# Kernel tuning notes

Measured on AMD Instinct MI355X. Metric: run time of the kernel, lower is better.

The kernel has to match this reference:

```python
import jax, jax.numpy as jnp
import numpy as np

N, E = 10000, 160000
D, H, C, FF, L = 128, 4, 32, 512, 2
INNER = H * C
VOCAB, RELVOCAB = 32000, 100
EPS = 1e-6
GATE_BIAS = 3.0


def _layer_norm(x, w, b):
    mu = jnp.mean(x, axis=-1, keepdims=True)
    var = jnp.mean(jnp.square(x - mu), axis=-1, keepdims=True)
    return (x - mu) * jax.lax.rsqrt(var + EPS) * w + b


def setup_inputs() -> dict:
    key = jax.random.key(0)
    ks = jax.random.split(key, 24)
    s = 1.0 / np.sqrt(D)
    inp = {
        "node_ids": jax.random.randint(ks[0], (N,), 0, VOCAB),
        "edge_index": jax.random.randint(ks[1], (2, E), 0, N),
        "edge_ids": jax.random.randint(ks[2], (E,), 0, RELVOCAB),
        "node_emb": jax.random.normal(ks[3], (VOCAB, D), jnp.float32),
        "edge_emb": jax.random.normal(ks[4], (RELVOCAB, D), jnp.float32),
        # per-layer stacked params (torch Linear weight layout [out, in])
        "ln_w": jnp.ones((L, D), jnp.float32),
        "ln_b": jnp.zeros((L, D), jnp.float32),
        "q_w": jax.random.normal(ks[5], (L, INNER, D), jnp.float32) * (1.0 / np.sqrt(D * C)),
        "relA_w": jax.random.normal(ks[6], (L, FF, 2 * D), jnp.float32) * s,
        "relA_b": jnp.zeros((L, FF), jnp.float32),
        "relB_w": jax.random.normal(ks[7], (L, D, FF), jnp.float32) * s,
        "relB_b": jnp.zeros((L, D), jnp.float32),
        "relG_w": jax.random.normal(ks[8], (L, D, FF), jnp.float32) * s,
        "relG_b": jnp.zeros((L, D), jnp.float32),
        "k_w": jax.random.normal(ks[9], (L, INNER, 2 * D), jnp.float32) * s,
        "v_w": jax.random.normal(ks[10], (L, INNER, D), jnp.float32) * s,
        "o_w": jax.random.normal(ks[11], (L, D, INNER), jnp.float32) * (1.0 / np.sqrt(INNER)),
        "ff_ln_w": jnp.ones((L, D), jnp.float32),
        "ff_ln_b": jnp.zeros((L, D), jnp.float32),
        "wi_w": jax.random.normal(ks[12], (L, FF, D), jnp.float32) * s,
        "wo_w": jax.random.normal(ks[13], (L, D, FF), jnp.float32) * (1.0 / np.sqrt(FF)),
    }
    return inp


def _forward(node_ids, edge_index, edge_ids, node_emb, edge_emb, ln_w, ln_b,
             q_w, relA_w, relA_b, relB_w, relB_b, relG_w, relG_b,
             k_w, v_w, o_w, ff_ln_w, ff_ln_b, wi_w, wo_w):
    x = node_emb[node_ids]          # [N, D]
    ef = edge_emb[edge_ids]         # [E, D]
    src = edge_index[0]             # j (source / kv side)
    dst = edge_index[1]             # i (target / query side)
    for l in range(L):
        # --- relational self-attention ---
        q = _layer_norm(x, ln_w[l], ln_b[l])
        q = (q @ q_w[l].T).reshape(N, H, C)
        kv_j = x[src]                                   # [E, D]
        cat = jnp.concatenate([kv_j, ef], axis=-1)      # [E, 2D]
        inter = jax.nn.celu(cat @ relA_w[l].T + relA_b[l])   # [E, FF]
        gate = jax.nn.sigmoid(inter @ relG_w[l].T + relG_b[l] + GATE_BIAS)
        k_add = inter @ relB_w[l].T + relB_b[l]
        kv2 = kv_j * gate + k_add * (1.0 - gate)        # [E, D]
        k = (jnp.concatenate([kv2, ef], axis=-1) @ k_w[l].T).reshape(E, H, C)
        v = (kv2 @ v_w[l].T).reshape(E, H, C)
        scores = jnp.sum(q[dst] * k, axis=-1)           # [E, H]
        smax = jax.ops.segment_max(scores, dst, num_segments=N)
        ex = jnp.exp(scores - smax[dst])
        denom = jax.ops.segment_sum(ex, dst, num_segments=N)
        alpha = ex / denom[dst]                         # [E, H]
        msg = (v * alpha[..., None]).reshape(E, INNER)
        agg = jax.ops.segment_sum(msg, dst, num_segments=N)  # [N, INNER]
        x = x + agg @ o_w[l].T
        # --- feed-forward (T5-style, pre-LN, relu, residual) ---
        h = _layer_norm(x, ff_ln_w[l], ff_ln_b[l])
        x = x + jax.nn.relu(h @ wi_w[l].T) @ wo_w[l].T
    return x


def reference(node_ids, edge_index, edge_ids, node_emb, edge_emb, ln_w, ln_b,
              q_w, relA_w, relA_b, relB_w, relB_b, relG_w, relG_b,
              k_w, v_w, o_w, ff_ln_w, ff_ln_b, wi_w, wo_w):
    return _forward(node_ids, edge_index, edge_ids, node_emb, edge_emb, ln_w, ln_b,
                    q_w, relA_w, relA_b, relB_w, relB_b, relG_w, relG_b,
                    k_w, v_w, o_w, ff_ln_w, ff_ln_b, wi_w, wo_w)
```

## Files before the change

kernel.cpp:

```cpp
#include <hip/hip_runtime.h>
#include <hip/hip_bf16.h>

#define NN 10000
#define EE 160000
#define DD 128
#define HH 4
#define CC 32
#define FFF 512
#define LL 2
#define RELV 100
#define EPS 1e-6f
#define GATE_BIAS 3.0f
#define BM 32
#define NT 16

typedef __bf16 bf16x8 __attribute__((ext_vector_type(8)));
typedef float f32x4 __attribute__((ext_vector_type(4)));
typedef float f32x16 __attribute__((ext_vector_type(16)));

#define MFMA(a,b,c)   __builtin_amdgcn_mfma_f32_16x16x32_bf16((a),(b),(c),0,0,0)
#define MFMA32(a,b,c) __builtin_amdgcn_mfma_f32_32x32x16_bf16((a),(b),(c),0,0,0)

__device__ __forceinline__ int swzK(int e, int b){ return e*256 + (b ^ ((e&7)<<4)); }
__device__ __forceinline__ int swz128(int e, int b){ return e*256 + (b ^ ((e&7)<<4)); }
__device__ __forceinline__ int swz512(int e, int b){ return e*1024 + (b ^ ((e&7)<<4)); }

__global__ __launch_bounds__(256) void k_gx(
    const int* __restrict__ node_ids, const float* __restrict__ node_emb,
    float* __restrict__ x, ushort* __restrict__ xb,
    const int* __restrict__ dst, int* __restrict__ hist){
  int b = blockIdx.x, t = threadIdx.x;
  int n = b*2 + (t>>7);
  int c = t & 127;
  float v = node_emb[(long)node_ids[n]*DD + c];
  x[(long)n*DD + c] = v;
  __hip_bfloat16 h = __float2bfloat16(v);
  xb[(long)n*DD + c] = *(ushort*)&h;
  if (t < 32){
    int e = b*32 + t;
    atomicAdd(&hist[dst[e]], 1);
  }
}

__device__ __forceinline__ void wprep_one(
    const float* __restrict__ in, ushort* __restrict__ out, int tid, int IN, int instride){
  int lane = tid & 63;
  int grp  = tid >> 6;
  int nkb  = IN >> 4;
  int kb   = grp % nkb;
  int cb   = grp / nkb;
  int col  = cb*32 + (lane & 31);
  int k0   = kb*16 + (lane >> 5)*8;
  const float* p = in + (long)col*instride + k0;
  bf16x8 h;
  #pragma unroll
  for (int j=0;j<8;++j) h[j] = (__bf16)p[j];
  *(bf16x8*)(out + (long)tid*8) = h;
}

__global__ __launch_bounds__(256) void k_prep(
    const float* __restrict__ relG_w, const float* __restrict__ relB_w,
    const float* __restrict__ k_w, const float* __restrict__ v_w,
    const float* __restrict__ relA_w,
    ushort* __restrict__ Gwb, ushort* __restrict__ Bwb,
    ushort* __restrict__ Kwb, ushort* __restrict__ Vwb, ushort* __restrict__ A1b){
  int tid = blockIdx.x*256 + threadIdx.x;
  if (tid < DD*FFF/8){
    wprep_one(relG_w, Gwb, tid, FFF, FFF);
    wprep_one(relB_w, Bwb, tid, FFF, FFF);
  }
  if (tid < DD*DD/8){
    wprep_one(k_w, Kwb, tid, DD, 256);
    wprep_one(v_w, Vwb, tid, DD, DD);
  }
  {
    int o = tid / DD, i = tid % DD;
    __hip_bfloat16 h = __float2bfloat16(relA_w[(long)o*256 + i]);
    A1b[tid] = *(ushort*)&h;
  }
}

__global__ __launch_bounds__(256) void k_f2b4(
    const float* __restrict__ q_w, const float* __restrict__ o_w,
    const float* __restrict__ wi_w, const float* __restrict__ wo_w,
    ushort* __restrict__ Qwb, ushort* __restrict__ Owb,
    ushort* __restrict__ Wib, ushort* __restrict__ Wob){
  long i = (long)blockIdx.x*256 + threadIdx.x;
  const long nV = (long)LL*DD*DD;
  if (i < nV){
    __hip_bfloat16 h1 = __float2bfloat16(q_w[i]); Qwb[i] = *(ushort*)&h1;
    __hip_bfloat16 h2 = __float2bfloat16(o_w[i]); Owb[i] = *(ushort*)&h2;
  }
  {
    __hip_bfloat16 h3 = __float2bfloat16(wi_w[i]); Wib[i] = *(ushort*)&h3;
    __hip_bfloat16 h4 = __float2bfloat16(wo_w[i]); Wob[i] = *(ushort*)&h4;
  }
}

__global__ __launch_bounds__(256) void k_ea(
    const float* __restrict__ edge_emb, const float* __restrict__ relA_w,
    const float* __restrict__ relA_b, const float* __restrict__ k_w,
    ushort* __restrict__ EA2b, float* __restrict__ EKf){
  int rel = blockIdx.x, t = threadIdx.x;
  __shared__ float emb[128];
  if (t < 128) emb[t] = edge_emb[(long)rel*DD + t];
  __syncthreads();
  for (int f=t; f<FFF; f+=256){
    const float* wr = relA_w + (long)f*256 + 128;
    float s = relA_b[f];
    for (int i=0;i<128;++i) s += emb[i]*wr[i];
    __hip_bfloat16 h = __float2bfloat16(s);
    EA2b[(long)rel*FFF + f] = *(ushort*)&h;
  }
  if (t < 128){
    const float* wr = k_w + (long)t*256 + 128;
    float s = 0.f;
    for (int i=0;i<128;++i) s += emb[i]*wr[i];
    EKf[(long)rel*DD + t] = s;
  }
}

__global__ __launch_bounds__(256) void k_scan(const int* __restrict__ hist, int* __restrict__ cursor){
  __shared__ int tsum[256];
  const int t = threadIdx.x;
  const int PER = (NN + 255) / 256;
  const int base = t*PER;
  int s = 0;
  for (int i=0;i<PER;++i){ int idx = base+i; if (idx < NN) s += hist[idx]; }
  tsum[t] = s;
  __syncthreads();
  if (t == 0){
    int run = 0;
    for (int i=0;i<256;++i){ int v = tsum[i]; tsum[i] = run; run += v; }
  }
  __syncthreads();
  int run = tsum[t];
  for (int i=0;i<PER;++i){
    int idx = base+i;
    if (idx < NN){ int v = hist[idx]; cursor[idx] = run; run += v; }
  }
}
__global__ __launch_bounds__(256) void k_scatter(const int* __restrict__ dst,
    int* __restrict__ cursor, int* __restrict__ perm){
  int e = blockIdx.x*256 + threadIdx.x;
  if (e < EE){
    int p = atomicAdd(&cursor[dst[e]], 1);
    perm[p] = e;
  }
}

__global__ __launch_bounds__(256) void k_lnq_xa(
    const float* __restrict__ x, const float* __restrict__ lnw, const float* __restrict__ lnb,
    const ushort* __restrict__ qwb, const ushort* __restrict__ a1b,
    float* __restrict__ q, ushort* __restrict__ XAb,
    float* __restrict__ agg, float* __restrict__ denom){
  __shared__ __align__(16) unsigned char HB[NT*256];
  __shared__ __align__(16) unsigned char HR[NT*256];
  const int n0 = blockIdx.x*NT;
  const int t = threadIdx.x;
  const int e = t>>4, s = t&15;
  const int w = t>>6, l = t&63, lr = l&15, lg = l>>4;
  {
    float4 z4 = {0.f,0.f,0.f,0.f};
    float* ap = agg + (long)n0*DD + t*8;
    *(float4*)ap = z4; *(float4*)(ap+4) = z4;
    if (t < NT*HH) denom[n0*HH + t] = 0.f;
  }
  {
    const float* xp = x + (long)(n0+e)*DD + s*8;
    float xv[8];
    *(float4*)&xv[0] = *(const float4*)xp;
    *(float4*)&xv[4] = *(const float4*)(xp+4);
    float sm = 0.f;
    #pragma unroll
    for (int i=0;i<8;++i) sm += xv[i];
    sm += __shfl_xor(sm,1); sm += __shfl_xor(sm,2);
    sm += __shfl_xor(sm,4); sm += __shfl_xor(sm,8);
    float mu = sm*(1.f/DD);
    float sq = 0.f;
    #pragma unroll
    for (int i=0;i<8;++i){ float d = xv[i]-mu; sq += d*d; }
    sq += __shfl_xor(sq,1); sq += __shfl_xor(sq,2);
    sq += __shfl_xor(sq,4); sq += __shfl_xor(sq,8);
    float rstd = rsqrtf(sq*(1.f/DD) + EPS);
    float4 w0 = *(const float4*)(lnw + s*8), w1 = *(const float4*)(lnw + s*8 + 4);
    float4 b0 = *(const float4*)(lnb + s*8), b1 = *(const float4*)(lnb + s*8 + 4);
    float wv[8] = {w0.x,w0.y,w0.z,w0.w,w1.x,w1.y,w1.z,w1.w};
    float bv[8] = {b0.x,b0.y,b0.z,b0.w,b1.x,b1.y,b1.z,b1.w};
    bf16x8 hb, hr;
    #pragma unroll
    for (int i=0;i<8;++i){
      hb[i] = (__bf16)((xv[i]-mu)*rstd*wv[i] + bv[i]);
      hr[i] = (__bf16)xv[i];
    }
    *(bf16x8*)(HB + swz128(e, s*16)) = hb;
    *(bf16x8*)(HR + swz128(e, s*16)) = hr;
  }
  __syncthreads();
  {
    const int o0 = w*32;
    f32x4 z = {0.f,0.f,0.f,0.f};
    f32x4 acc[2] = {z,z};
    #pragma unroll
    for (int k4=0;k4<4;++k4){
      bf16x8 a = *(const bf16x8*)(HB + swz128(lr, k4*64 + lg*16));
      #pragma unroll
      for (int nt=0;nt<2;++nt){
        bf16x8 b = *(const bf16x8*)(qwb + (long)(o0+nt*16+lr)*128 + k4*32 + lg*8);
        acc[nt] = MFMA(a, b, acc[nt]);
      }
    }
    #pragma unroll
    for (int nt=0;nt<2;++nt)
      #pragma unroll
      for (int r=0;r<4;++r)
        q[(long)(n0 + lg*4 + r)*DD + o0 + nt*16 + lr] = acc[nt][r];
  }
  {
    const int f0w = w*128;
    f32x4 z = {0.f,0.f,0.f,0.f};
    f32x4 acc[8] = {z,z,z,z,z,z,z,z};
    #pragma unroll
    for (int k4=0;k4<4;++k4){
      bf16x8 a = *(const bf16x8*)(HR + swz128(lr, k4*64 + lg*16));
      #pragma unroll
      for (int nt=0;nt<8;++nt){
        bf16x8 b = *(const bf16x8*)(a1b + (long)(f0w+nt*16+lr)*128 + k4*32 + lg*8);
        acc[nt] = MFMA(a, b, acc[nt]);
      }
    }
    #pragma unroll
    for (int nt=0;nt<8;++nt)
      #pragma unroll
      for (int r=0;r<4;++r){
        __hip_bfloat16 h = __float2bfloat16(acc[nt][r]);
        XAb[(long)(n0+lg*4+r)*FFF + f0w+nt*16+lr] = *(ushort*)&h;
      }
  }
}

__global__ __launch_bounds__(256,4) void k_edge(
    const ushort* __restrict__ xb, const ushort* __restrict__ XAb,
    const ushort* __restrict__ EAb, const float* __restrict__ EKf,
    const float* __restrict__ q,
    const int* __restrict__ src, const int* __restrict__ dst, const int* __restrict__ eids,
    const int* __restrict__ perm,
    const ushort* __restrict__ Gwb, const float* __restrict__ Gb,
    const ushort* __restrict__ Bwb, const float* __restrict__ Bb,
    const ushort* __restrict__ Kwb, const ushort* __restrict__ Vwb,
    float* __restrict__ agg, float* __restrict__ denom)
{
  __shared__ __align__(16) unsigned char KVB[BM*256];
  __shared__ __align__(16) unsigned char INTB[2][BM*256];
  __shared__ int srcl[BM], dstl[BM], eidl[BM];

  int nb;
  {
    const int cpx = (EE/BM) >> 3;
    nb = (blockIdx.x & 7)*cpx + (blockIdx.x >> 3);
  }
  const int e0 = nb * BM;
  const int t  = threadIdx.x;
  const int w  = t >> 6;
  const int l  = t & 63;
  const int c32 = l & 31;
  const int hi  = l >> 5;
  const int C = w;
  const int oc = C*32 + c32;

  if (t < BM){
    int pe = perm[e0+t];
    srcl[t] = src[pe]; dstl[t] = dst[pe]; eidl[t] = eids[pe];
  }
  __syncthreads();

  {
    const uint4* xbu = (const uint4*)xb;
    #pragma unroll
    for (int it=0; it<2; ++it){
      int g = it*256 + t;
      int e = g >> 4, qq = g & 15;
      *(uint4*)(KVB + swzK(e, qq*16)) = xbu[(long)srcl[e]*16 + qq];
    }
  }

  f32x16 gbG, gbB;
  {
    float bg = Gb[oc] + GATE_BIAS;
    float bb = Bb[oc];
    #pragma unroll
    for (int i=0;i<16;++i){ gbG[i] = bg; gbB[i] = bb; }
  }

  bf16x8 xa8[2], ea8[2];
  #pragma unroll
  for (int it=0; it<2; ++it){
    int g = it*256 + t;
    int e = g >> 4, c8 = g & 15;
    xa8[it] = *(const bf16x8*)(XAb + (long)srcl[e]*FFF + c8*8);
    ea8[it] = *(const bf16x8*)(EAb + (long)eidl[e]*FFF + c8*8);
  }

  #pragma unroll
  for (int ch=0; ch<4; ++ch){
    bf16x8 o[2];
    #pragma unroll
    for (int it=0; it<2; ++it){
      #pragma unroll
      for (int j=0;j<8;++j){
        float s = (float)xa8[it][j] + (float)ea8[it][j];
        o[it][j] = (__bf16)((s > 0.f) ? s : (__expf(s) - 1.f));
      }
    }
    unsigned char* INTp = INTB[ch & 1];
    #pragma unroll
    for (int it=0; it<2; ++it){
      int g = it*256 + t;
      int e = g >> 4, c8 = g & 15;
      *(bf16x8*)(INTp + swzK(e, c8*16)) = o[it];
    }
    __syncthreads();
    if (ch < 3){
      #pragma unroll
      for (int it=0; it<2; ++it){
        int g = it*256 + t;
        int e = g >> 4, c8 = g & 15;
        xa8[it] = *(const bf16x8*)(XAb + (long)srcl[e]*FFF + (ch+1)*128 + c8*8);
        ea8[it] = *(const bf16x8*)(EAb + (long)eidl[e]*FFF + (ch+1)*128 + c8*8);
      }
    }
    {
      const ushort* Wg = Gwb + ((long)(C*32 + ch*8)*64 + l)*8;
      bf16x8 wf[8];
      #pragma unroll
      for (int i=0;i<8;++i) wf[i] = *(const bf16x8*)(Wg + (long)i*512);
      #pragma unroll
      for (int i=0;i<8;++i){
        bf16x8 a = *(const bf16x8*)(INTp + swzK(c32, i*32 + hi*16));
        gbG = MFMA32(a, wf[i], gbG);
      }
    }
    {
      const ushort* Wb = Bwb + ((long)(C*32 + ch*8)*64 + l)*8;
      bf16x8 wf[8];
      #pragma unroll
      for (int i=0;i<8;++i) wf[i] = *(const bf16x8*)(Wb + (long)i*512);
      #pragma unroll
      for (int i=0;i<8;++i){
        bf16x8 a = *(const bf16x8*)(INTp + swzK(c32, i*32 + hi*16));
        gbB = MFMA32(a, wf[i], gbB);
      }
    }
  }

  #pragma unroll
  for (int r=0;r<16;++r){
    int row = (r&3) + 8*(r>>2) + 4*hi;
    float g  = 1.f/(1.f + __expf(-gbG[r]));
    float kv = (float)*(const __bf16*)(KVB + swzK(row, oc*2));
    float k2 = gbB[r] + g*(kv - gbB[r]);
    *(__bf16*)(KVB + swzK(row, oc*2)) = (__bf16)k2;
  }
  __syncthreads();

  f32x16 ka, va;
  #pragma unroll
  for (int i=0;i<16;++i){ ka[i] = 0.f; va[i] = 0.f; }
  {
    const ushort* Wk = Kwb + ((long)(C*8)*64 + l)*8;
    bf16x8 wf[8];
    #pragma unroll
    for (int i=0;i<8;++i) wf[i] = *(const bf16x8*)(Wk + (long)i*512);
    #pragma unroll
    for (int i=0;i<8;++i){
      bf16x8 a = *(const bf16x8*)(KVB + swzK(c32, i*32 + hi*16));
      ka = MFMA32(a, wf[i], ka);
    }
  }
  {
    const ushort* Wv = Vwb + ((long)(C*8)*64 + l)*8;
    bf16x8 wf[8];
    #pragma unroll
    for (int i=0;i<8;++i) wf[i] = *(const bf16x8*)(Wv + (long)i*512);
    #pragma unroll
    for (int i=0;i<8;++i){
      bf16x8 a = *(const bf16x8*)(KVB + swzK(c32, i*32 + hi*16));
      va = MFMA32(a, wf[i], va);
    }
  }

  #pragma unroll
  for (int qq=0; qq<4; ++qq){
    const int base = 8*qq + 4*hi;
    float ex[4];
    #pragma unroll
    for (int j=0;j<4;++j){
      int r = qq*4 + j;
      int gr = base + j;
      float kv = ka[r] + EKf[(long)eidl[gr]*DD + oc];
      float p = kv * q[(long)dstl[gr]*DD + oc];
      p += __shfl_xor(p, 1); p += __shfl_xor(p, 2);
      p += __shfl_xor(p, 4); p += __shfl_xor(p, 8);
      p += __shfl_xor(p, 16);
      ex[j] = __expf(p);
    }
    {
      float acc = va[qq*4]*ex[0];
      int cur = dstl[base];
      #pragma unroll
      for (int j=1;j<4;++j){
        int dn = dstl[base+j];
        if (dn != cur){
          atomicAdd(&agg[(long)cur*DD + oc], acc);
          acc = 0.f; cur = dn;
        }
        acc += va[qq*4+j]*ex[j];
      }
      atomicAdd(&agg[(long)cur*DD + oc], acc);
    }
    if (c32 == 0){
      float da = ex[0];
      int cur = dstl[base];
      #pragma unroll
      for (int j=1;j<4;++j){
        int dn = dstl[base+j];
        if (dn != cur){
          atomicAdd(&denom[cur*HH + C], da);
          da = 0.f; cur = dn;
        }
        da += ex[j];
      }
      atomicAdd(&denom[cur*HH + C], da);
    }
  }
}

template<bool FUSE_LNQ>
__global__ __launch_bounds__(256) void k_node(
    const float* __restrict__ agg, const float* __restrict__ denom,
    const ushort* __restrict__ owb,
    const float* __restrict__ lnw, const float* __restrict__ lnb,
    const ushort* __restrict__ wib, const ushort* __restrict__ wob,
    float* __restrict__ x, ushort* __restrict__ xb,
    const float* __restrict__ nlnw, const float* __restrict__ nlnb,
    const ushort* __restrict__ nqwb, const ushort* __restrict__ na1b,
    float* __restrict__ q, ushort* __restrict__ XAb){
  __shared__ __align__(16) unsigned char AB[NT*256];
  __shared__ __align__(16) unsigned char IB[NT*1024];
  __shared__ __align__(16) float XO[NT][132];
  const int n0 = blockIdx.x*NT;
  const int t = threadIdx.x;
  const int e = t>>4, s = t&15;
  const int w = t>>6, l = t&63, lr = l&15, lg = l>>4;

  {
    const float* ap = agg + (long)(n0+e)*DD + s*8;
    float av[8];
    *(float4*)&av[0] = *(const float4*)ap;
    *(float4*)&av[4] = *(const float4*)(ap+4);
    float dinv = 1.f / denom[(n0+e)*HH + (s>>2)];
    bf16x8 hb;
    #pragma unroll
    for (int i=0;i<8;++i) hb[i] = (__bf16)(av[i]*dinv);
    *(bf16x8*)(AB + swz128(e, s*16)) = hb;
  }
  __syncthreads();

  {
    const int o0 = w*32;
    f32x4 z = {0.f,0.f,0.f,0.f};
    f32x4 acc[2] = {z,z};
    #pragma unroll
    for (int k4=0;k4<4;++k4){
      bf16x8 a = *(const bf16x8*)(AB + swz128(lr, k4*64 + lg*16));
      #pragma unroll
      for (int nt=0;nt<2;++nt){
        bf16x8 b = *(const bf16x8*)(owb + (long)(o0+nt*16+lr)*128 + k4*32 + lg*8);
        acc[nt] = MFMA(a, b, acc[nt]);
      }
    }
    #pragma unroll
    for (int nt=0;nt<2;++nt)
      #pragma unroll
      for (int r=0;r<4;++r)
        XO[lg*4+r][o0+nt*16+lr] = acc[nt][r];
  }
  __syncthreads();

  float x1[8];
  {
    const float* xp = x + (long)(n0+e)*DD + s*8;
    float xv[8];
    *(float4*)&xv[0] = *(const float4*)xp;
    *(float4*)&xv[4] = *(const float4*)(xp+4);
    #pragma unroll
    for (int i=0;i<8;++i) x1[i] = xv[i] + XO[e][s*8+i];
    float sm = 0.f;
    #pragma unroll
    for (int i=0;i<8;++i) sm += x1[i];
    sm += __shfl_xor(sm,1); sm += __shfl_xor(sm,2);
    sm += __shfl_xor(sm,4); sm += __shfl_xor(sm,8);
    float mu = sm*(1.f/DD);
    float sq = 0.f;
    #pragma unroll
    for (int i=0;i<8;++i){ float d = x1[i]-mu; sq += d*d; }
    sq += __shfl_xor(sq,1); sq += __shfl_xor(sq,2);
    sq += __shfl_xor(sq,4); sq += __shfl_xor(sq,8);
    float rstd = rsqrtf(sq*(1.f/DD) + EPS);
    float4 w0 = *(const float4*)(lnw + s*8), w1 = *(const float4*)(lnw + s*8 + 4);
    float4 b0 = *(const float4*)(lnb + s*8), b1 = *(const float4*)(lnb + s*8 + 4);
    float wv[8] = {w0.x,w0.y,w0.z,w0.w,w1.x,w1.y,w1.z,w1.w};
    float bv[8] = {b0.x,b0.y,b0.z,b0.w,b1.x,b1.y,b1.z,b1.w};
    bf16x8 hb;
    #pragma unroll
    for (int i=0;i<8;++i) hb[i] = (__bf16)((x1[i]-mu)*rstd*wv[i] + bv[i]);
    __syncthreads();
    *(bf16x8*)(AB + swz128(e, s*16)) = hb;
  }
  __syncthreads();

  {
    const int f0w = w*128;
    f32x4 z = {0.f,0.f,0.f,0.f};
    f32x4 acc[8] = {z,z,z,z,z,z,z,z};
    #pragma unroll
    for (int k4=0;k4<4;++k4){
      bf16x8 a = *(const bf16x8*)(AB + swz128(lr, k4*64 + lg*16));
      #pragma unroll
      for (int nt=0;nt<8;++nt){
        bf16x8 b = *(const bf16x8*)(wib + (long)(f0w+nt*16+lr)*128 + k4*32 + lg*8);
        acc[nt] = MFMA(a, b, acc[nt]);
      }
    }
    #pragma unroll
    for (int nt=0;nt<8;++nt)
      #pragma unroll
      for (int r=0;r<4;++r){
        int e2 = lg*4 + r;
        int f = f0w + nt*16 + lr;
        float va = acc[nt][r];
        *(__bf16*)(IB + swz512(e2, f*2)) = (__bf16)fmaxf(va, 0.f);
      }
  }
  __syncthreads();

  {
    const int o0 = w*32;
    f32x4 z = {0.f,0.f,0.f,0.f};
    f32x4 acc[2] = {z,z};
    #pragma unroll
    for (int k16=0;k16<16;++k16){
      bf16x8 a = *(const bf16x8*)(IB + swz512(lr, k16*64 + lg*16));
      #pragma unroll
      for (int nt=0;nt<2;++nt){
        bf16x8 b = *(const bf16x8*)(wob + (long)(o0+nt*16+lr)*512 + k16*32 + lg*8);
        acc[nt] = MFMA(a, b, acc[nt]);
      }
    }
    #pragma unroll
    for (int nt=0;nt<2;++nt)
      #pragma unroll
      for (int r=0;r<4;++r)
        XO[lg*4+r][o0+nt*16+lr] = acc[nt][r];
  }
  __syncthreads();

  float xn[8];
  {
    #pragma unroll
    for (int i=0;i<8;++i) xn[i] = x1[i] + XO[e][s*8+i];
    float* xp = x + (long)(n0+e)*DD + s*8;
    *(float4*)xp = *(float4*)&xn[0];
    *(float4*)(xp+4) = *(float4*)&xn[4];
    bf16x8 hb;
    #pragma unroll
    for (int i=0;i<8;++i) hb[i] = (__bf16)xn[i];
    *(bf16x8*)(xb + (long)(n0+e)*DD + s*8) = hb;
  }

  if constexpr (FUSE_LNQ){
    {
      float4 z4 = {0.f,0.f,0.f,0.f};
      float* ap = (float*)agg + (long)n0*DD + t*8;
      *(float4*)ap = z4; *(float4*)(ap+4) = z4;
      if (t < NT*HH) ((float*)denom)[n0*HH + t] = 0.f;
    }
    {
      float sm = 0.f;
      #pragma unroll
      for (int i=0;i<8;++i) sm += xn[i];
      sm += __shfl_xor(sm,1); sm += __shfl_xor(sm,2);
      sm += __shfl_xor(sm,4); sm += __shfl_xor(sm,8);
      float mu = sm*(1.f/DD);
      float sq = 0.f;
      #pragma unroll
      for (int i=0;i<8;++i){ float d = xn[i]-mu; sq += d*d; }
      sq += __shfl_xor(sq,1); sq += __shfl_xor(sq,2);
      sq += __shfl_xor(sq,4); sq += __shfl_xor(sq,8);
      float rstd = rsqrtf(sq*(1.f/DD) + EPS);
      float4 w0 = *(const float4*)(nlnw + s*8), w1 = *(const float4*)(nlnw + s*8 + 4);
      float4 b0 = *(const float4*)(nlnb + s*8), b1 = *(const float4*)(nlnb + s*8 + 4);
      float wv[8] = {w0.x,w0.y,w0.z,w0.w,w1.x,w1.y,w1.z,w1.w};
      float bv[8] = {b0.x,b0.y,b0.z,b0.w,b1.x,b1.y,b1.z,b1.w};
      bf16x8 hb, hr;
      #pragma unroll
      for (int i=0;i<8;++i){
        hb[i] = (__bf16)((xn[i]-mu)*rstd*wv[i] + bv[i]);
        hr[i] = (__bf16)xn[i];
      }
      *(bf16x8*)(AB + swz128(e, s*16)) = hb;
      *(bf16x8*)(IB + swz128(e, s*16)) = hr;
    }
    __syncthreads();
    {
      const int o0 = w*32;
      f32x4 z = {0.f,0.f,0.f,0.f};
      f32x4 acc[2] = {z,z};
      #pragma unroll
      for (int k4=0;k4<4;++k4){
        bf16x8 a = *(const bf16x8*)(AB + swz128(lr, k4*64 + lg*16));
        #pragma unroll
        for (int nt=0;nt<2;++nt){
          bf16x8 b = *(const bf16x8*)(nqwb + (long)(o0+nt*16+lr)*128 + k4*32 + lg*8);
          acc[nt] = MFMA(a, b, acc[nt]);
        }
      }
      #pragma unroll
      for (int nt=0;nt<2;++nt)
        #pragma unroll
        for (int r=0;r<4;++r)
          q[(long)(n0 + lg*4 + r)*DD + o0 + nt*16 + lr] = acc[nt][r];
    }
    {
      const int f0w = w*128;
      f32x4 z = {0.f,0.f,0.f,0.f};
      f32x4 acc[8] = {z,z,z,z,z,z,z,z};
      #pragma unroll
      for (int k4=0;k4<4;++k4){
        bf16x8 a = *(const bf16x8*)(IB + swz128(lr, k4*64 + lg*16));
        #pragma unroll
        for (int nt=0;nt<8;++nt){
          bf16x8 b = *(const bf16x8*)(na1b + (long)(f0w+nt*16+lr)*128 + k4*32 + lg*8);
          acc[nt] = MFMA(a, b, acc[nt]);
        }
      }
      #pragma unroll
      for (int nt=0;nt<8;++nt)
        #pragma unroll
        for (int r=0;r<4;++r){
          __hip_bfloat16 h = __float2bfloat16(acc[nt][r]);
          XAb[(long)(n0+lg*4+r)*FFF + f0w+nt*16+lr] = *(ushort*)&h;
        }
    }
  }
}

extern "C" void kernel_launch(void* const* d_in, const int* in_sizes, int n_in,
                              void* d_out, int out_size, void* d_ws, size_t ws_size,
                              hipStream_t stream) {
  const int* node_ids   = (const int*)d_in[0];
  const int* edge_index = (const int*)d_in[1];
  const int* edge_ids   = (const int*)d_in[2];
  const float* node_emb = (const float*)d_in[3];
  const float* edge_emb = (const float*)d_in[4];
  const float* ln_w   = (const float*)d_in[5];
  const float* ln_b   = (const float*)d_in[6];
  const float* q_w    = (const float*)d_in[7];
  const float* relA_w = (const float*)d_in[8];
  const float* relA_b = (const float*)d_in[9];
  const float* relB_w = (const float*)d_in[10];
  const float* relB_b = (const float*)d_in[11];
  const float* relG_w = (const float*)d_in[12];
  const float* relG_b = (const float*)d_in[13];
  const float* k_w    = (const float*)d_in[14];
  const float* v_w    = (const float*)d_in[15];
  const float* o_w    = (const float*)d_in[16];
  const float* ff_ln_w= (const float*)d_in[17];
  const float* ff_ln_b= (const float*)d_in[18];
  const float* wi_w   = (const float*)d_in[19];
  const float* wo_w   = (const float*)d_in[20];
  const int* src = edge_index;
  const int* dst = edge_index + EE;

  float* ws = (float*)d_ws;
  float* x   = ws;  ws += (long)NN*DD;
  float* q   = ws;  ws += (long)NN*DD;
  float* denom = ws; ws += NN*HH;
  float* agg   = ws; ws += (long)NN*DD;
  float* EKf   = ws; ws += (long)LL*RELV*DD;
  int* hist   = (int*)ws; ws += NN;
  int* perm   = (int*)ws; ws += EE;
  ushort* xb  = (ushort*)ws; ws += (long)NN*DD/2;
  ushort* XAb = (ushort*)ws; ws += (long)NN*FFF/2;
  ushort* EAb = (ushort*)ws; ws += (long)LL*RELV*FFF/2;
  ushort* A1b = (ushort*)ws; ws += (long)LL*FFF*DD/2;
  ushort* Gwb = (ushort*)ws; ws += (long)LL*DD*FFF/2;
  ushort* Bwb = (ushort*)ws; ws += (long)LL*DD*FFF/2;
  ushort* Kwb = (ushort*)ws; ws += (long)LL*DD*DD/2;
  ushort* Vwb = (ushort*)ws; ws += (long)LL*DD*DD/2;
  ushort* Qwb = (ushort*)ws; ws += (long)LL*DD*DD/2;
  ushort* Owb = (ushort*)ws; ws += (long)LL*DD*DD/2;
  ushort* Wib = (ushort*)ws; ws += (long)LL*FFF*DD/2;
  ushort* Wob = (ushort*)ws; ws += (long)LL*DD*FFF/2;

  hipMemsetAsync(hist, 0, NN*sizeof(int), stream);
  k_gx<<<NN/2, 256, 0, stream>>>(node_ids, node_emb, x, xb, dst, hist);
  k_scan<<<1, 256, 0, stream>>>(hist, hist);
  k_scatter<<<(EE+255)/256, 256, 0, stream>>>(dst, hist, perm);
  for (int l=0; l<LL; ++l){
    k_prep<<<256, 256, 0, stream>>>(
        relG_w + (long)l*DD*FFF, relB_w + (long)l*DD*FFF,
        k_w + (long)l*DD*256,    v_w + (long)l*DD*DD,
        relA_w + (long)l*FFF*256,
        Gwb + (long)l*DD*FFF, Bwb + (long)l*DD*FFF,
        Kwb + (long)l*DD*DD,  Vwb + (long)l*DD*DD, A1b + (long)l*FFF*DD);
    k_ea<<<RELV, 256, 0, stream>>>(edge_emb, relA_w + (long)l*FFF*256, relA_b + (long)l*FFF,
                                   k_w + (long)l*DD*256, EAb + (long)l*RELV*FFF, EKf + (long)l*RELV*DD);
  }
  k_f2b4<<<512, 256, 0, stream>>>(q_w, o_w, wi_w, wo_w, Qwb, Owb, Wib, Wob);

  k_lnq_xa<<<NN/NT, 256, 0, stream>>>(x, ln_w, ln_b, Qwb, A1b, q, XAb, agg, denom);
  for (int l=0; l<LL; ++l){
    k_edge<<<EE/BM, 256, 0, stream>>>(xb, XAb, EAb + (long)l*RELV*FFF, EKf + (long)l*RELV*DD,
        q, src, dst, edge_ids, perm,
        Gwb + (long)l*DD*FFF,  relG_b + (long)l*DD,
        Bwb + (long)l*DD*FFF,  relB_b + (long)l*DD,
        Kwb + (long)l*DD*DD,   Vwb + (long)l*DD*DD,
        agg, denom);
    if (l < LL-1){
      k_node<true><<<NN/NT, 256, 0, stream>>>(agg, denom, Owb + (long)l*DD*DD,
          ff_ln_w + l*DD, ff_ln_b + l*DD,
          Wib + (long)l*FFF*DD, Wob + (long)l*DD*FFF, x, xb,
          ln_w + (l+1)*DD, ln_b + (l+1)*DD,
          Qwb + (long)(l+1)*DD*DD, A1b + (long)(l+1)*FFF*DD, q, XAb);
    } else {
      k_node<false><<<NN/NT, 256, 0, stream>>>(agg, denom, Owb + (long)l*DD*DD,
          ff_ln_w + l*DD, ff_ln_b + l*DD,
          Wib + (long)l*FFF*DD, Wob + (long)l*DD*FFF, x, xb,
          nullptr, nullptr, nullptr, nullptr, nullptr, nullptr);
    }
  }
  hipMemcpyAsync(d_out, x, (size_t)NN*DD*sizeof(float), hipMemcpyDeviceToDevice, stream);
}
```

Baseline: 426.1 us.

## Merge weight-prep launches and process relation MLP in two 256-wide chunks

Folds the per-layer weight conversion kernels and the fp32-to-bf16 cast kernel into a single launch, and runs the relation-embedding kernel for both layers in one grid, cutting five launches down to two. In the edge kernel, the 512-wide ELU intermediate is staged in two 256-column halves using one larger shared buffer instead of four 128-column double-buffered chunks. This halves the number of block barriers and chunk iterations, but doubles the in-flight gather registers. It also adds a barrier to protect the reused buffer.

New measurement: 421.0 us. Within noise of the previous version (-1.2%).

```diff
diff --git a/kernel.cpp b/kernel.cpp
--- a/kernel.cpp
+++ b/kernel.cpp
@@ -22,6 +22,7 @@
 #define MFMA32(a,b,c) __builtin_amdgcn_mfma_f32_32x32x16_bf16((a),(b),(c),0,0,0)
 
 __device__ __forceinline__ int swzK(int e, int b){ return e*256 + (b ^ ((e&7)<<4)); }
+__device__ __forceinline__ int swzI(int e, int b){ return e*512 + (b ^ ((e&7)<<4)); }
 __device__ __forceinline__ int swz128(int e, int b){ return e*256 + (b ^ ((e&7)<<4)); }
 __device__ __forceinline__ int swz512(int e, int b){ return e*1024 + (b ^ ((e&7)<<4)); }
 
@@ -58,65 +59,68 @@
   *(bf16x8*)(out + (long)tid*8) = h;
 }
 
-__global__ __launch_bounds__(256) void k_prep(
+__global__ __launch_bounds__(256) void k_prep2(
     const float* __restrict__ relG_w, const float* __restrict__ relB_w,
     const float* __restrict__ k_w, const float* __restrict__ v_w,
     const float* __restrict__ relA_w,
-    ushort* __restrict__ Gwb, ushort* __restrict__ Bwb,
-    ushort* __restrict__ Kwb, ushort* __restrict__ Vwb, ushort* __restrict__ A1b){
-  int tid = blockIdx.x*256 + threadIdx.x;
-  if (tid < DD*FFF/8){
-    wprep_one(relG_w, Gwb, tid, FFF, FFF);
-    wprep_one(relB_w, Bwb, tid, FFF, FFF);
-  }
-  if (tid < DD*DD/8){
-    wprep_one(k_w, Kwb, tid, DD, 256);
-    wprep_one(v_w, Vwb, tid, DD, DD);
-  }
-  {
-    int o = tid / DD, i = tid % DD;
-    __hip_bfloat16 h = __float2bfloat16(relA_w[(long)o*256 + i]);
-    A1b[tid] = *(ushort*)&h;
-  }
-}
-
-__global__ __launch_bounds__(256) void k_f2b4(
     const float* __restrict__ q_w, const float* __restrict__ o_w,
     const float* __restrict__ wi_w, const float* __restrict__ wo_w,
+    ushort* __restrict__ Gwb, ushort* __restrict__ Bwb,
+    ushort* __restrict__ Kwb, ushort* __restrict__ Vwb, ushort* __restrict__ A1b,
     ushort* __restrict__ Qwb, ushort* __restrict__ Owb,
     ushort* __restrict__ Wib, ushort* __restrict__ Wob){
-  long i = (long)blockIdx.x*256 + threadIdx.x;
-  const long nV = (long)LL*DD*DD;
-  if (i < nV){
-    __hip_bfloat16 h1 = __float2bfloat16(q_w[i]); Qwb[i] = *(ushort*)&h1;
-    __hip_bfloat16 h2 = __float2bfloat16(o_w[i]); Owb[i] = *(ushort*)&h2;
-  }
-  {
-    __hip_bfloat16 h3 = __float2bfloat16(wi_w[i]); Wib[i] = *(ushort*)&h3;
-    __hip_bfloat16 h4 = __float2bfloat16(wo_w[i]); Wob[i] = *(ushort*)&h4;
-  }
-}
-
-__global__ __launch_bounds__(256) void k_ea(
+  const int bid = blockIdx.x;
+  const int l   = bid >> 8;
+  const int tidl = (bid & 255)*256 + threadIdx.x;
+  const long gid = (long)bid*256 + threadIdx.x;
+  if (tidl < DD*FFF/8){
+    wprep_one(relG_w + (long)l*DD*FFF, Gwb + (long)l*DD*FFF, tidl, FFF, FFF);
+    wprep_one(relB_w + (long)l*DD*FFF, Bwb + (long)l*DD*FFF, tidl, FFF, FFF);
+  }
+  if (tidl < DD*DD/8){
+    wprep_one(k_w + (long)l*DD*256, Kwb + (long)l*DD*DD, tidl, DD, 256);
+    wprep_one(v_w + (long)l*DD*DD,  Vwb + (long)l*DD*DD, tidl, DD, DD);
+  }
+  {
+    int o = tidl / DD, i = tidl % DD;
+    __hip_bfloat16 h = __float2bfloat16(relA_w[(long)l*FFF*256 + (long)o*256 + i]);
+    A1b[(long)l*FFF*DD + tidl] = *(ushort*)&h;
+  }
+  if (gid < (long)LL*DD*DD){
+    __hip_bfloat16 h1 = __float2bfloat16(q_w[gid]); Qwb[gid] = *(ushort*)&h1;
+    __hip_bfloat16 h2 = __float2bfloat16(o_w[gid]); Owb[gid] = *(ushort*)&h2;
+  }
+  {
+    __hip_bfloat16 h3 = __float2bfloat16(wi_w[gid]); Wib[gid] = *(ushort*)&h3;
+    __hip_bfloat16 h4 = __float2bfloat16(wo_w[gid]); Wob[gid] = *(ushort*)&h4;
+  }
+}
+
+__global__ __launch_bounds__(256) void k_ea2(
     const float* __restrict__ edge_emb, const float* __restrict__ relA_w,
     const float* __restrict__ relA_b, const float* __restrict__ k_w,
     ushort* __restrict__ EA2b, float* __restrict__ EKf){
-  int rel = blockIdx.x, t = threadIdx.x;
+  int l = blockIdx.x / RELV, rel = blockIdx.x % RELV, t = threadIdx.x;
+  const float* Aw = relA_w + (long)l*FFF*256;
+  const float* Ab = relA_b + (long)l*FFF;
+  const float* Kw = k_w + (long)l*DD*256;
+  ushort* EAo = EA2b + (long)l*RELV*FFF;
+  float* EKo  = EKf + (long)l*RELV*DD;
   __shared__ float emb[128];
   if (t < 128) emb[t] = edge_emb[(long)rel*DD + t];
   __syncthreads();
   for (int f=t; f<FFF; f+=256){
-    const float* wr = relA_w + (long)f*256 + 128;
-    float s = relA_b[f];
+    const float* wr = Aw + (long)f*256 + 128;
+    float s = Ab[f];
     for (int i=0;i<128;++i) s += emb[i]*wr[i];
     __hip_bfloat16 h = __float2bfloat16(s);
-    EA2b[(long)rel*FFF + f] = *(ushort*)&h;
+    EAo[(long)rel*FFF + f] = *(ushort*)&h;
   }
   if (t < 128){
-    const float* wr = k_w + (long)t*256 + 128;
+    const float* wr = Kw + (long)t*256 + 128;
     float s = 0.f;
     for (int i=0;i<128;++i) s += emb[i]*wr[i];
-    EKf[(long)rel*DD + t] = s;
+    EKo[(long)rel*DD + t] = s;
   }
 }
 
@@ -251,7 +255,7 @@
     float* __restrict__ agg, float* __restrict__ denom)
 {
   __shared__ __align__(16) unsigned char KVB[BM*256];
-  __shared__ __align__(16) unsigned char INTB[2][BM*256];
+  __shared__ __align__(16) unsigned char INTB[BM*512];
   __shared__ int srcl[BM], dstl[BM], eidl[BM];
 
   int nb;
@@ -292,65 +296,68 @@
     for (int i=0;i<16;++i){ gbG[i] = bg; gbB[i] = bb; }
   }
 
-  bf16x8 xa8[2], ea8[2];
+  bf16x8 xa8[4], ea8[4];
   #pragma unroll
-  for (int it=0; it<2; ++it){
+  for (int it=0; it<4; ++it){
     int g = it*256 + t;
-    int e = g >> 4, c8 = g & 15;
+    int e = g >> 5, c8 = g & 31;
     xa8[it] = *(const bf16x8*)(XAb + (long)srcl[e]*FFF + c8*8);
     ea8[it] = *(const bf16x8*)(EAb + (long)eidl[e]*FFF + c8*8);
   }
 
   #pragma unroll
-  for (int ch=0; ch<4; ++ch){
-    bf16x8 o[2];
-    #pragma unroll
-    for (int it=0; it<2; ++it){
+  for (int ch=0; ch<2; ++ch){
+    #pragma unroll
+    for (int it=0; it<4; ++it){
+      bf16x8 o;
       #pragma unroll
       for (int j=0;j<8;++j){
         float s = (float)xa8[it][j] + (float)ea8[it][j];
-        o[it][j] = (__bf16)((s > 0.f) ? s : (__expf(s) - 1.f));
-      }
-    }
-    unsigned char* INTp = INTB[ch & 1];
-    #pragma unroll
-    for (int it=0; it<2; ++it){
+        o[j] = (__bf16)((s > 0.f) ? s : (__expf(s) - 1.f));
+      }
       int g = it*256 + t;
-      int e = g >> 4, c8 = g & 15;
-      *(bf16x8*)(INTp + swzK(e, c8*16)) = o[it];
+      int e = g >> 5, c8 = g & 31;
+      *(bf16x8*)(INTB + swzI(e, c8*16)) = o;
     }
     __syncthreads();
-    if (ch < 3){
-      #pragma unroll
-      for (int it=0; it<2; ++it){
+    if (ch == 0){
+      #pragma unroll
+      for (int it=0; it<4; ++it){
         int g = it*256 + t;
-        int e = g >> 4, c8 = g & 15;
-        xa8[it] = *(const bf16x8*)(XAb + (long)srcl[e]*FFF + (ch+1)*128 + c8*8);
-        ea8[it] = *(const bf16x8*)(EAb + (long)eidl[e]*FFF + (ch+1)*128 + c8*8);
+        int e = g >> 5, c8 = g & 31;
+        xa8[it] = *(const bf16x8*)(XAb + (long)srcl[e]*FFF + 256 + c8*8);
+        ea8[it] = *(const bf16x8*)(EAb + (long)eidl[e]*FFF + 256 + c8*8);
       }
     }
     {
-      const ushort* Wg = Gwb + ((long)(C*32 + ch*8)*64 + l)*8;
-      bf16x8 wf[8];
-      #pragma unroll
-      for (int i=0;i<8;++i) wf[i] = *(const bf16x8*)(Wg + (long)i*512);
-      #pragma unroll
-      for (int i=0;i<8;++i){
-        bf16x8 a = *(const bf16x8*)(INTp + swzK(c32, i*32 + hi*16));
-        gbG = MFMA32(a, wf[i], gbG);
+      const ushort* Wg = Gwb + ((long)(C*32 + ch*16)*64 + l)*8;
+      #pragma unroll
+      for (int h2=0; h2<2; ++h2){
+        bf16x8 wf[8];
+        #pragma unroll
+        for (int i=0;i<8;++i) wf[i] = *(const bf16x8*)(Wg + (long)(h2*8+i)*512);
+        #pragma unroll
+        for (int i=0;i<8;++i){
+          bf16x8 a = *(const bf16x8*)(INTB + swzI(c32, (h2*8+i)*32 + hi*16));
+          gbG = MFMA32(a, wf[i], gbG);
+        }
       }
     }
     {
-      const ushort* Wb = Bwb + ((long)(C*32 + ch*8)*64 + l)*8;
-      bf16x8 wf[8];
-      #pragma unroll
-      for (int i=0;i<8;++i) wf[i] = *(const bf16x8*)(Wb + (long)i*512);
-      #pragma unroll
-      for (int i=0;i<8;++i){
-        bf16x8 a = *(const bf16x8*)(INTp + swzK(c32, i*32 + hi*16));
-        gbB = MFMA32(a, wf[i], gbB);
-      }
-    }
+      const ushort* Wb = Bwb + ((long)(C*32 + ch*16)*64 + l)*8;
+      #pragma unroll
+      for (int h2=0; h2<2; ++h2){
+        bf16x8 wf[8];
+        #pragma unroll
+        for (int i=0;i<8;++i) wf[i] = *(const bf16x8*)(Wb + (long)(h2*8+i)*512);
+        #pragma unroll
+        for (int i=0;i<8;++i){
+          bf16x8 a = *(const bf16x8*)(INTB + swzI(c32, (h2*8+i)*32 + hi*16));
+          gbB = MFMA32(a, wf[i], gbB);
+        }
+      }
+    }
+    if (ch == 0) __syncthreads();
   }
 
   #pragma unroll
@@ -707,17 +714,10 @@
   k_gx<<<NN/2, 256, 0, stream>>>(node_ids, node_emb, x, xb, dst, hist);
   k_scan<<<1, 256, 0, stream>>>(hist, hist);
   k_scatter<<<(EE+255)/256, 256, 0, stream>>>(dst, hist, perm);
-  for (int l=0; l<LL; ++l){
-    k_prep<<<256, 256, 0, stream>>>(
-        relG_w + (long)l*DD*FFF, relB_w + (long)l*DD*FFF,
-        k_w + (long)l*DD*256,    v_w + (long)l*DD*DD,
-        relA_w + (long)l*FFF*256,
-        Gwb + (long)l*DD*FFF, Bwb + (long)l*DD*FFF,
-        Kwb + (long)l*DD*DD,  Vwb + (long)l*DD*DD, A1b + (long)l*FFF*DD);
-    k_ea<<<RELV, 256, 0, stream>>>(edge_emb, relA_w + (long)l*FFF*256, relA_b + (long)l*FFF,
-                                   k_w + (long)l*DD*256, EAb + (long)l*RELV*FFF, EKf + (long)l*RELV*DD);
-  }
-  k_f2b4<<<512, 256, 0, stream>>>(q_w, o_w, wi_w, wo_w, Qwb, Owb, Wib, Wob);
+  k_prep2<<<512, 256, 0, stream>>>(relG_w, relB_w, k_w, v_w, relA_w,
+                                   q_w, o_w, wi_w, wo_w,
+                                   Gwb, Bwb, Kwb, Vwb, A1b, Qwb, Owb, Wib, Wob);
+  k_ea2<<<2*RELV, 256, 0, stream>>>(edge_emb, relA_w, relA_b, k_w, EAb, EKf);
 
   k_lnq_xa<<<NN/NT, 256, 0, stream>>>(x, ln_w, ln_b, Qwb, A1b, q, XAb, agg, denom);
   for (int l=0; l<LL; ++l){
```
